# Kernel tuning notes

Measured on AMD Instinct MI355X. Metric: run time of the kernel, lower is better.

The kernel has to match this reference:

```python
import jax, jax.numpy as jnp
import numpy as np

N_AGENT = 32768   # number of agent (dst) nodes
MAX_NBRS = 16     # fixed neighbor count per agent (pad target)
N_NBR = N_AGENT * MAX_NBRS   # nbr (src) nodes
E = N_AGENT * MAX_NBRS       # 1hop edges (grouped by dst)
F_NBR, F_AGENT, F_HOP = 32, 32, 8
H = 128           # critic_hidden_size
N_POW = 4         # n_pow_opts


def _lin(key, fin, fout):
    return jax.random.normal(key, (fin, fout), jnp.float32) / np.sqrt(fin)


def setup_inputs() -> dict:
    key = jax.random.key(0)
    ks = jax.random.split(key, 12)
    return {
        "feat_nbr": jax.random.normal(ks[0], (N_NBR, F_NBR), jnp.float32),
        "feat_agent": jax.random.normal(ks[1], (N_AGENT, F_AGENT), jnp.float32),
        "edge_feat": jax.random.normal(ks[2], (E, F_HOP), jnp.float32),
        "h": jnp.zeros((N_AGENT, H), jnp.float32),
        # NodeGNBlock '1hop': message MLP + update MLP
        "W_msg": _lin(ks[3], F_NBR + F_HOP, H), "b_msg": jnp.zeros((H,), jnp.float32),
        "W_upd": _lin(ks[4], H + F_AGENT, H), "b_upd": jnp.zeros((H,), jnp.float32),
        # RnnLayer: GRUCell(H, H)
        "W_x": _lin(ks[5], H, 3 * H), "W_h": _lin(ks[6], H, 3 * H),
        "b_ih": jnp.zeros((3 * H,), jnp.float32), "b_hh": jnp.zeros((3 * H,), jnp.float32),
        # EdgeGNBlock f_out: edge MLP -> per-edge q over power options, plus agent head
        "W_e1": _lin(ks[7], F_NBR + H + F_HOP, H), "b_e1": jnp.zeros((H,), jnp.float32),
        "W_e2": _lin(ks[8], H, N_POW), "b_e2": jnp.zeros((N_POW,), jnp.float32),
        "W_a": _lin(ks[9], 2 * H, 1), "b_a": jnp.zeros((1,), jnp.float32),
        # graph: each agent has exactly MAX_NBRS incident edges, grouped by dst
        "src_idx": jax.random.randint(ks[10], (E,), 0, N_NBR),
        "dst_idx": jnp.repeat(jnp.arange(N_AGENT), MAX_NBRS),
    }


def reference(feat_nbr, feat_agent, edge_feat, h,
              W_msg, b_msg, W_upd, b_upd,
              W_x, W_h, b_ih, b_hh,
              W_e1, b_e1, W_e2, b_e2, W_a, b_a,
              src_idx, dst_idx):
    act = jax.nn.relu
    # --- NodeGNBlock '1hop': edge message -> sum-aggregate -> node update ---
    m = act(jnp.concatenate([feat_nbr[src_idx], edge_feat], axis=1) @ W_msg + b_msg)  # [E,H]
    agg = jax.ops.segment_sum(m, dst_idx, num_segments=N_AGENT, indices_are_sorted=True)  # [N,H]
    x = act(jnp.concatenate([agg, feat_agent], axis=1) @ W_upd + b_upd)  # [N,H]
    # --- RnnLayer: GRUCell step; output x == new hidden ---
    gi = x @ W_x + b_ih
    gh = h @ W_h + b_hh
    ir, iz, inn = jnp.split(gi, 3, axis=1)
    hr, hz, hn = jnp.split(gh, 3, axis=1)
    r = jax.nn.sigmoid(ir + hr)
    z = jax.nn.sigmoid(iz + hz)
    n = jnp.tanh(inn + r * hn)
    h_new = (1.0 - z) * n + z * h  # [N,H]
    # --- EdgeGNBlock f_out: per-edge q-values + per-agent scalar ---
    ze = act(jnp.concatenate([feat_nbr[src_idx], h_new[dst_idx], edge_feat], axis=1) @ W_e1 + b_e1)  # [E,H]
    nbr_out = ze @ W_e2 + b_e2  # [E, N_POW]
    agg2 = jax.ops.segment_sum(ze, dst_idx, num_segments=N_AGENT, indices_are_sorted=True)
    agent_out = jnp.concatenate([agg2, h_new], axis=1) @ W_a + b_a  # [N,1]
    # --- pad_edge_output: edges grouped by dst with fixed degree -> reshape ---
    padded_nbr_out = nbr_out.reshape(N_AGENT, MAX_NBRS * N_POW)
    q_vals = jnp.concatenate([padded_nbr_out, agent_out], axis=1)  # [N, MAX_NBRS*N_POW+1]
    return q_vals, h_new
```

## Files before the change

kernel.cpp:

```cpp
#include <hip/hip_runtime.h>

typedef _Float16 half_t;
typedef half_t half8 __attribute__((ext_vector_type(8)));
typedef half_t half4 __attribute__((ext_vector_type(4)));
typedef float f32x4 __attribute__((ext_vector_type(4)));

#define NAGENT 32768
#define MAXN   16
#define HD     128
#define QCOLS  65
#define QN     (NAGENT * QCOLS)
#define AGB    16
#define EPB    (AGB * MAXN)
#define QROWB  260

#define O_WMT   0
#define O_WE1E  8192
#define O_WE1H  16384
#define O_WUPD  32768
#define O_WX    53248
#define O_WH    102400
#define W_TOTAL 151552

#define MFMA(a, b, c) __builtin_amdgcn_mfma_f32_16x16x32_f16((a), (b), (c), 0, 0, 0)

__global__ void prep_weights(const float* __restrict__ W_msg, const float* __restrict__ W_upd,
                             const float* __restrict__ W_x, const float* __restrict__ W_h,
                             const float* __restrict__ W_e1, half_t* __restrict__ ws) {
    int i = blockIdx.x * 256 + threadIdx.x;
    if (i >= W_TOTAL) return;
    float v; int dst;
    if (i < 8192) {
        int k = i >> 7, n = i & 127;
        v = (k < 40) ? W_msg[k * HD + n] : 0.f;
        dst = O_WMT + n * 64 + k;
    } else if (i < 16384) {
        int j = i - 8192; int k = j >> 7, n = j & 127;
        v = (k < 32) ? W_e1[k * HD + n] : (k < 40 ? W_e1[(160 + k - 32) * HD + n] : 0.f);
        dst = O_WE1E + n * 64 + k;
    } else if (i < 32768) {
        int j = i - 16384; int k = j >> 7, n = j & 127;
        v = W_e1[(32 + k) * HD + n];
        dst = O_WE1H + n * 128 + k;
    } else if (i < 53248) {
        int j = i - 32768; int k = j >> 7, n = j & 127;
        v = W_upd[k * HD + n];
        dst = O_WUPD + n * 160 + k;
    } else if (i < 102400) {
        int j = i - 53248; int k = j / 384, n = j - k * 384;
        v = W_x[k * 384 + n];
        dst = O_WX + n * 128 + k;
    } else {
        int j = i - 102400; int k = j / 384, n = j - k * 384;
        v = W_h[k * 384 + n];
        dst = O_WH + n * 128 + k;
    }
    ws[dst] = (half_t)v;
}

__device__ __forceinline__ half8 ldB(const half_t* __restrict__ WT, int kstride, int n0, int k0, int l) {
    return *(const half8*)(WT + (size_t)(n0 + (l & 15)) * kstride + k0 + ((l >> 4) * 8));
}
__device__ __forceinline__ half4 cvt4(float4 v) {
    return (half4){(half_t)v.x, (half_t)v.y, (half_t)v.z, (half_t)v.w};
}
__device__ __forceinline__ half8 cvt8(float4 a, float4 b) {
    return (half8){(half_t)a.x, (half_t)a.y, (half_t)a.z, (half_t)a.w,
                   (half_t)b.x, (half_t)b.y, (half_t)b.z, (half_t)b.w};
}
__device__ __forceinline__ float sigm(float x) { return 1.f / (1.f + __expf(-x)); }
__device__ __forceinline__ float tanh_fast(float x) { return 1.f - 2.f / (__expf(2.f * x) + 1.f); }

__global__ __launch_bounds__(256, 2) void k_msg(
    const float* __restrict__ feat_nbr, const float* __restrict__ edge_feat,
    const float* __restrict__ b_msg, const int* __restrict__ src_idx,
    const half_t* __restrict__ ws, float* __restrict__ out)
{
    const int t = threadIdx.x;
    const int w = t >> 6, l = t & 63;
    const int l16 = l & 15, q = l >> 4;
    const int a0 = blockIdx.x * AGB;
    const int be = blockIdx.x * EPB;
    const half_t* wmT = ws + O_WMT;
    const half8 hz = {0, 0, 0, 0, 0, 0, 0, 0};

    __shared__ int srcs[EPB];
    srcs[t] = src_idx[be + t];
    __syncthreads();

    half8 B[4][4];
    float bm0[4], bm1[4];
    #pragma unroll
    for (int nc = 0; nc < 4; ++nc) {
        const int n0 = nc * 32;
        B[nc][0] = ldB(wmT, 64, n0, 0, l);
        B[nc][1] = ldB(wmT, 64, n0, 32, l);
        B[nc][2] = ldB(wmT, 64, n0 + 16, 0, l);
        B[nc][3] = ldB(wmT, 64, n0 + 16, 32, l);
        bm0[nc] = b_msg[n0 + l16];
        bm1[nc] = b_msg[n0 + 16 + l16];
    }
    #pragma unroll
    for (int mt = 0; mt < 4; ++mt) {
        const int al = w * 4 + mt;
        const int arow = al * 16 + l16;
        const float* fr = feat_nbr + (size_t)srcs[arow] * 32 + q * 8;
        half8 af0 = cvt8(*(const float4*)fr, *(const float4*)(fr + 4));
        half8 af1 = hz;
        if (q == 0) {
            const float* er = edge_feat + (size_t)(be + arow) * 8;
            af1 = cvt8(*(const float4*)er, *(const float4*)(er + 4));
        }
        half_t* arow_out = (half_t*)((char*)out + (size_t)(a0 + al) * QROWB);
        #pragma unroll
        for (int nc = 0; nc < 4; ++nc) {
            f32x4 c0 = {0.f, 0.f, 0.f, 0.f}, c1 = {0.f, 0.f, 0.f, 0.f};
            c0 = MFMA(af0, B[nc][0], c0);
            c0 = MFMA(af1, B[nc][1], c0);
            c1 = MFMA(af0, B[nc][2], c1);
            c1 = MFMA(af1, B[nc][3], c1);
            float s0 = 0.f, s1 = 0.f;
            #pragma unroll
            for (int r = 0; r < 4; ++r) {
                s0 += fmaxf(c0[r] + bm0[nc], 0.f);
                s1 += fmaxf(c1[r] + bm1[nc], 0.f);
            }
            s0 += __shfl_xor(s0, 16); s0 += __shfl_xor(s0, 32);
            s1 += __shfl_xor(s1, 16); s1 += __shfl_xor(s1, 32);
            if (l < 16) {
                arow_out[nc * 32 + l] = (half_t)s0;
                arow_out[nc * 32 + 16 + l] = (half_t)s1;
            }
        }
    }
}

__global__ __launch_bounds__(256, 2) void k_node(
    const float* __restrict__ feat_agent, const float* __restrict__ h_in,
    const float* __restrict__ b_upd, const float* __restrict__ b_ih,
    const float* __restrict__ b_hh, const float* __restrict__ b_e1,
    const float* __restrict__ W_a, half_t* __restrict__ ws,
    float* __restrict__ out)
{
    const int t = threadIdx.x;
    const int w = t >> 6, l = t & 63;
    const int l16 = l & 15, q = l >> 4;
    const int a0 = blockIdx.x * AGB;
    const half_t* wupdT = ws + O_WUPD;
    const half_t* wxT   = ws + O_WX;
    const half_t* whT   = ws + O_WH;
    const half_t* we1hT = ws + O_WE1H;
    float* hn_wa_g = (float*)(ws + W_TOTAL);

    __shared__ half_t A2[AGB][168];
    __shared__ half_t h_lds[AGB][136];
    __shared__ half_t x_lds[AGB][136];
    __shared__ half_t hn_lds[AGB][136];
    __shared__ float  hnwa[AGB];

    if (t < AGB) hnwa[t] = 0.f;
    {
        int r = t >> 4, c = t & 15;
        half8 v = *(const half8*)((const char*)out + (size_t)(a0 + r) * QROWB + c * 16);
        *(half8*)&A2[r][c * 8] = v;
    }
    if (t < 128) {
        int r = t >> 3, p = t & 7;
        float4 v = ((const float4*)(feat_agent + (size_t)(a0 + r) * 32))[p];
        *(half4*)&A2[r][128 + p * 4] = cvt4(v);
    }
    #pragma unroll
    for (int i = 0; i < 2; ++i) {
        int g = t + 256 * i; int r = g >> 5, c = g & 31;
        float4 v = ((const float4*)(h_in + (size_t)(a0 + r) * HD))[c];
        *(half4*)&h_lds[r][c * 4] = cvt4(v);
    }
    __syncthreads();

    {
        half8 af[5];
        #pragma unroll
        for (int k = 0; k < 5; ++k) af[k] = *(const half8*)&A2[l16][k * 32 + q * 8];
        #pragma unroll
        for (int s = 0; s < 2; ++s) {
            const int n0 = (w * 2 + s) * 16;
            f32x4 c = {0.f, 0.f, 0.f, 0.f};
            #pragma unroll
            for (int k = 0; k < 5; ++k) c = MFMA(af[k], ldB(wupdT, 160, n0, k * 32, l), c);
            float bu = b_upd[n0 + l16];
            #pragma unroll
            for (int r = 0; r < 4; ++r)
                x_lds[q * 4 + r][n0 + l16] = (half_t)fmaxf(c[r] + bu, 0.f);
        }
    }
    __syncthreads();

    {
        half8 ax[4], ah[4];
        #pragma unroll
        for (int k = 0; k < 4; ++k) {
            ax[k] = *(const half8*)&x_lds[l16][k * 32 + q * 8];
            ah[k] = *(const half8*)&h_lds[l16][k * 32 + q * 8];
        }
        float pa[4] = {0.f, 0.f, 0.f, 0.f};
        #pragma unroll
        for (int s = 0; s < 2; ++s) {
            const int colb = w * 32 + s * 16;
            f32x4 gi[3], gh[3];
            #pragma unroll
            for (int g = 0; g < 3; ++g) {
                const int n0 = g * 128 + colb;
                f32x4 ci = {0.f, 0.f, 0.f, 0.f}, ch = {0.f, 0.f, 0.f, 0.f};
                #pragma unroll
                for (int k = 0; k < 4; ++k) {
                    ci = MFMA(ax[k], ldB(wxT, 128, n0, k * 32, l), ci);
                    ch = MFMA(ah[k], ldB(whT, 128, n0, k * 32, l), ch);
                }
                gi[g] = ci; gh[g] = ch;
            }
            const int col = colb + l16;
            float bi0 = b_ih[col], bi1 = b_ih[HD + col], bi2 = b_ih[2 * HD + col];
            float bh0 = b_hh[col], bh1 = b_hh[HD + col], bh2 = b_hh[2 * HD + col];
            float wac = W_a[HD + col];
            #pragma unroll
            for (int r = 0; r < 4; ++r) {
                const int row = q * 4 + r;
                float rg = sigm(gi[0][r] + bi0 + gh[0][r] + bh0);
                float zg = sigm(gi[1][r] + bi1 + gh[1][r] + bh1);
                float ng = tanh_fast(gi[2][r] + bi2 + rg * (gh[2][r] + bh2));
                float hv = (1.f - zg) * ng + zg * (float)h_lds[row][col];
                out[QN + (size_t)(a0 + row) * HD + col] = hv;
                hn_lds[row][col] = (half_t)hv;
                pa[r] = fmaf(hv, wac, pa[r]);
            }
        }
        #pragma unroll
        for (int r = 0; r < 4; ++r) {
            #pragma unroll
            for (int m = 1; m <= 8; m <<= 1) pa[r] += __shfl_xor(pa[r], m);
            if (l16 == 0) atomicAdd(&hnwa[q * 4 + r], pa[r]);
        }
    }
    __syncthreads();

    {
        half8 an[4];
        #pragma unroll
        for (int k = 0; k < 4; ++k) an[k] = *(const half8*)&hn_lds[l16][k * 32 + q * 8];
        #pragma unroll
        for (int s = 0; s < 2; ++s) {
            const int n0 = (w * 2 + s) * 16;
            f32x4 c = {0.f, 0.f, 0.f, 0.f};
            #pragma unroll
            for (int k = 0; k < 4; ++k) c = MFMA(an[k], ldB(we1hT, 128, n0, k * 32, l), c);
            float bv = b_e1[n0 + l16];
            #pragma unroll
            for (int r = 0; r < 4; ++r) {
                half_t* arow_out = (half_t*)((char*)out + (size_t)(a0 + q * 4 + r) * QROWB);
                arow_out[n0 + l16] = (half_t)(c[r] + bv);
            }
        }
    }
    if (t < AGB) hn_wa_g[a0 + t] = hnwa[t];
}

__global__ __launch_bounds__(256, 2) void k_edge(
    const float* __restrict__ feat_nbr, const float* __restrict__ edge_feat,
    const float* __restrict__ W_e2, const float* __restrict__ b_e2,
    const float* __restrict__ W_a, const float* __restrict__ b_a,
    const int* __restrict__ src_idx, const half_t* __restrict__ ws,
    float* __restrict__ out)
{
    const int t = threadIdx.x;
    const int w = t >> 6, l = t & 63;
    const int l16 = l & 15, q = l >> 4;
    const int a0 = blockIdx.x * AGB;
    const int be = blockIdx.x * EPB;
    const half_t* we1eT = ws + O_WE1E;
    const float* hn_wa_g = (const float*)(ws + W_TOTAL);
    const half8 hz = {0, 0, 0, 0, 0, 0, 0, 0};

    __shared__ int srcs[EPB];
    srcs[t] = src_idx[be + t];
    __syncthreads();

    half8 B[4][4];
    float wa0[4], wa1[4];
    #pragma unroll
    for (int nc = 0; nc < 4; ++nc) {
        const int n0 = nc * 32;
        B[nc][0] = ldB(we1eT, 64, n0, 0, l);
        B[nc][1] = ldB(we1eT, 64, n0, 32, l);
        B[nc][2] = ldB(we1eT, 64, n0 + 16, 0, l);
        B[nc][3] = ldB(we1eT, 64, n0 + 16, 32, l);
        wa0[nc] = W_a[n0 + l16];
        wa1[nc] = W_a[n0 + 16 + l16];
    }
    const float ba = b_a[0];

    #pragma unroll
    for (int mt = 0; mt < 4; ++mt) {
        const int al = w * 4 + mt;
        const int arow = al * 16 + l16;
        const float* fr = feat_nbr + (size_t)srcs[arow] * 32 + q * 8;
        half8 af0 = cvt8(*(const float4*)fr, *(const float4*)(fr + 4));
        half8 af1 = hz;
        if (q == 0) {
            const float* er = edge_feat + (size_t)(be + arow) * 8;
            af1 = cvt8(*(const float4*)er, *(const float4*)(er + 4));
        }
        const half_t* che_row = (const half_t*)((const char*)out + (size_t)(a0 + al) * QROWB);
        float qa[4][4];
        #pragma unroll
        for (int r = 0; r < 4; ++r)
            #pragma unroll
            for (int p = 0; p < 4; ++p) qa[r][p] = 0.f;
        float wa_part = 0.f;
        #pragma unroll
        for (int nc = 0; nc < 4; ++nc) {
            const int n0 = nc * 32;
            f32x4 c0 = {0.f, 0.f, 0.f, 0.f}, c1 = {0.f, 0.f, 0.f, 0.f};
            c0 = MFMA(af0, B[nc][0], c0);
            c0 = MFMA(af1, B[nc][1], c0);
            c1 = MFMA(af0, B[nc][2], c1);
            c1 = MFMA(af1, B[nc][3], c1);
            const int col0 = n0 + l16, col1 = n0 + 16 + l16;
            float ch0 = (float)che_row[col0], ch1 = (float)che_row[col1];
            float4 w20 = *(const float4*)(W_e2 + col0 * 4);
            float4 w21 = *(const float4*)(W_e2 + col1 * 4);
            float s0 = 0.f, s1 = 0.f;
            #pragma unroll
            for (int r = 0; r < 4; ++r) {
                float z0 = fmaxf(c0[r] + ch0, 0.f);
                float z1 = fmaxf(c1[r] + ch1, 0.f);
                s0 += z0; s1 += z1;
                qa[r][0] = fmaf(z0, w20.x, fmaf(z1, w21.x, qa[r][0]));
                qa[r][1] = fmaf(z0, w20.y, fmaf(z1, w21.y, qa[r][1]));
                qa[r][2] = fmaf(z0, w20.z, fmaf(z1, w21.z, qa[r][2]));
                qa[r][3] = fmaf(z0, w20.w, fmaf(z1, w21.w, qa[r][3]));
            }
            s0 += __shfl_xor(s0, 16); s0 += __shfl_xor(s0, 32);
            s1 += __shfl_xor(s1, 16); s1 += __shfl_xor(s1, 32);
            wa_part = fmaf(s0, wa0[nc], fmaf(s1, wa1[nc], wa_part));
        }
        #pragma unroll
        for (int m = 1; m <= 8; m <<= 1)
            #pragma unroll
            for (int r = 0; r < 4; ++r)
                #pragma unroll
                for (int p = 0; p < 4; ++p) qa[r][p] += __shfl_xor(qa[r][p], m);
        if (l16 < 4) {
            const int p = l16;
            const float bz = b_e2[p];
            #pragma unroll
            for (int r = 0; r < 4; ++r)
                out[(size_t)(a0 + al) * QCOLS + (q * 4 + r) * 4 + p] = qa[r][p] + bz;
        }
        #pragma unroll
        for (int m = 1; m <= 8; m <<= 1) wa_part += __shfl_xor(wa_part, m);
        if (l == 0)
            out[(size_t)(a0 + al) * QCOLS + 64] = wa_part + hn_wa_g[a0 + al] + ba;
    }
}

extern "C" void kernel_launch(void* const* d_in, const int* in_sizes, int n_in,
                              void* d_out, int out_size, void* d_ws, size_t ws_size,
                              hipStream_t stream) {
    const float* feat_nbr   = (const float*)d_in[0];
    const float* feat_agent = (const float*)d_in[1];
    const float* edge_feat  = (const float*)d_in[2];
    const float* h_in       = (const float*)d_in[3];
    const float* W_msg = (const float*)d_in[4];
    const float* b_msg = (const float*)d_in[5];
    const float* W_upd = (const float*)d_in[6];
    const float* b_upd = (const float*)d_in[7];
    const float* W_x   = (const float*)d_in[8];
    const float* W_h   = (const float*)d_in[9];
    const float* b_ih  = (const float*)d_in[10];
    const float* b_hh  = (const float*)d_in[11];
    const float* W_e1  = (const float*)d_in[12];
    const float* b_e1  = (const float*)d_in[13];
    const float* W_e2  = (const float*)d_in[14];
    const float* b_e2  = (const float*)d_in[15];
    const float* W_a   = (const float*)d_in[16];
    const float* b_a   = (const float*)d_in[17];
    const int* src_idx = (const int*)d_in[18];
    half_t* ws = (half_t*)d_ws;
    float* out = (float*)d_out;
    const int nblk = NAGENT / AGB;

    prep_weights<<<(W_TOTAL + 255) / 256, 256, 0, stream>>>(W_msg, W_upd, W_x, W_h, W_e1, ws);
    k_msg<<<nblk, 256, 0, stream>>>(feat_nbr, edge_feat, b_msg, src_idx, ws, out);
    k_node<<<nblk, 256, 0, stream>>>(feat_agent, h_in, b_upd, b_ih, b_hh, b_e1, W_a, ws, out);
    k_edge<<<nblk, 256, 0, stream>>>(feat_nbr, edge_feat, W_e2, b_e2, W_a, b_a, src_idx, ws, out);
}
```

Baseline: 316.1 us.

## Fuse message, node/GRU and edge kernels into one per-block kernel

Merges the three per-block kernels (k_msg, k_node, k_edge) into a single kernel. Intermediates (aggregated messages, h_new projections, the hn·W_a partial) now stay in LDS instead of round-tripping through the output buffer and workspace. The gathered feat_nbr and edge_feat rows are cached in LDS as fp16 and reused by the edge stage, so the random gather happens once instead of twice. LDS buffers are aliased to limit shared memory, and launch bounds are raised to 3 blocks per CU. The risks are higher register and LDS pressure and a longer serial dependency chain within each block.

```diff
diff --git a/kernel.cpp b/kernel.cpp
--- a/kernel.cpp
+++ b/kernel.cpp
@@ -12,7 +12,6 @@
 #define QN     (NAGENT * QCOLS)
 #define AGB    16
 #define EPB    (AGB * MAXN)
-#define QROWB  260
 
 #define O_WMT   0
 #define O_WE1E  8192
@@ -71,9 +70,14 @@
 __device__ __forceinline__ float sigm(float x) { return 1.f / (1.f + __expf(-x)); }
 __device__ __forceinline__ float tanh_fast(float x) { return 1.f - 2.f / (__expf(2.f * x) + 1.f); }
 
-__global__ __launch_bounds__(256, 2) void k_msg(
-    const float* __restrict__ feat_nbr, const float* __restrict__ edge_feat,
-    const float* __restrict__ b_msg, const int* __restrict__ src_idx,
+__global__ __launch_bounds__(256, 3) void k_fused(
+    const float* __restrict__ feat_nbr, const float* __restrict__ feat_agent,
+    const float* __restrict__ edge_feat, const float* __restrict__ h_in,
+    const float* __restrict__ b_msg, const float* __restrict__ b_upd,
+    const float* __restrict__ b_ih, const float* __restrict__ b_hh,
+    const float* __restrict__ b_e1, const float* __restrict__ W_e2,
+    const float* __restrict__ b_e2, const float* __restrict__ W_a,
+    const float* __restrict__ b_a, const int* __restrict__ src_idx,
     const half_t* __restrict__ ws, float* __restrict__ out)
 {
     const int t = threadIdx.x;
@@ -81,93 +85,21 @@
     const int l16 = l & 15, q = l >> 4;
     const int a0 = blockIdx.x * AGB;
     const int be = blockIdx.x * EPB;
-    const half_t* wmT = ws + O_WMT;
     const half8 hz = {0, 0, 0, 0, 0, 0, 0, 0};
 
-    __shared__ int srcs[EPB];
+    __shared__ int    srcs[EPB];
+    __shared__ half_t fnef[EPB][40];
+    __shared__ half_t bufA[AGB][168];
+    __shared__ half_t h_lds[AGB][136];
+    __shared__ half_t bufB[AGB][136];
+    __shared__ float  hnwa[AGB];
+
     srcs[t] = src_idx[be + t];
-    __syncthreads();
-
-    half8 B[4][4];
-    float bm0[4], bm1[4];
-    #pragma unroll
-    for (int nc = 0; nc < 4; ++nc) {
-        const int n0 = nc * 32;
-        B[nc][0] = ldB(wmT, 64, n0, 0, l);
-        B[nc][1] = ldB(wmT, 64, n0, 32, l);
-        B[nc][2] = ldB(wmT, 64, n0 + 16, 0, l);
-        B[nc][3] = ldB(wmT, 64, n0 + 16, 32, l);
-        bm0[nc] = b_msg[n0 + l16];
-        bm1[nc] = b_msg[n0 + 16 + l16];
-    }
-    #pragma unroll
-    for (int mt = 0; mt < 4; ++mt) {
-        const int al = w * 4 + mt;
-        const int arow = al * 16 + l16;
-        const float* fr = feat_nbr + (size_t)srcs[arow] * 32 + q * 8;
-        half8 af0 = cvt8(*(const float4*)fr, *(const float4*)(fr + 4));
-        half8 af1 = hz;
-        if (q == 0) {
-            const float* er = edge_feat + (size_t)(be + arow) * 8;
-            af1 = cvt8(*(const float4*)er, *(const float4*)(er + 4));
-        }
-        half_t* arow_out = (half_t*)((char*)out + (size_t)(a0 + al) * QROWB);
-        #pragma unroll
-        for (int nc = 0; nc < 4; ++nc) {
-            f32x4 c0 = {0.f, 0.f, 0.f, 0.f}, c1 = {0.f, 0.f, 0.f, 0.f};
-            c0 = MFMA(af0, B[nc][0], c0);
-            c0 = MFMA(af1, B[nc][1], c0);
-            c1 = MFMA(af0, B[nc][2], c1);
-            c1 = MFMA(af1, B[nc][3], c1);
-            float s0 = 0.f, s1 = 0.f;
-            #pragma unroll
-            for (int r = 0; r < 4; ++r) {
-                s0 += fmaxf(c0[r] + bm0[nc], 0.f);
-                s1 += fmaxf(c1[r] + bm1[nc], 0.f);
-            }
-            s0 += __shfl_xor(s0, 16); s0 += __shfl_xor(s0, 32);
-            s1 += __shfl_xor(s1, 16); s1 += __shfl_xor(s1, 32);
-            if (l < 16) {
-                arow_out[nc * 32 + l] = (half_t)s0;
-                arow_out[nc * 32 + 16 + l] = (half_t)s1;
-            }
-        }
-    }
-}
-
-__global__ __launch_bounds__(256, 2) void k_node(
-    const float* __restrict__ feat_agent, const float* __restrict__ h_in,
-    const float* __restrict__ b_upd, const float* __restrict__ b_ih,
-    const float* __restrict__ b_hh, const float* __restrict__ b_e1,
-    const float* __restrict__ W_a, half_t* __restrict__ ws,
-    float* __restrict__ out)
-{
-    const int t = threadIdx.x;
-    const int w = t >> 6, l = t & 63;
-    const int l16 = l & 15, q = l >> 4;
-    const int a0 = blockIdx.x * AGB;
-    const half_t* wupdT = ws + O_WUPD;
-    const half_t* wxT   = ws + O_WX;
-    const half_t* whT   = ws + O_WH;
-    const half_t* we1hT = ws + O_WE1H;
-    float* hn_wa_g = (float*)(ws + W_TOTAL);
-
-    __shared__ half_t A2[AGB][168];
-    __shared__ half_t h_lds[AGB][136];
-    __shared__ half_t x_lds[AGB][136];
-    __shared__ half_t hn_lds[AGB][136];
-    __shared__ float  hnwa[AGB];
-
     if (t < AGB) hnwa[t] = 0.f;
-    {
-        int r = t >> 4, c = t & 15;
-        half8 v = *(const half8*)((const char*)out + (size_t)(a0 + r) * QROWB + c * 16);
-        *(half8*)&A2[r][c * 8] = v;
-    }
     if (t < 128) {
         int r = t >> 3, p = t & 7;
         float4 v = ((const float4*)(feat_agent + (size_t)(a0 + r) * 32))[p];
-        *(half4*)&A2[r][128 + p * 4] = cvt4(v);
+        *(half4*)&bufA[r][128 + p * 4] = cvt4(v);
     }
     #pragma unroll
     for (int i = 0; i < 2; ++i) {
@@ -178,9 +110,61 @@
     __syncthreads();
 
     {
+        const half_t* wmT = ws + O_WMT;
+        half8 B[4][4];
+        float bm0[4], bm1[4];
+        #pragma unroll
+        for (int nc = 0; nc < 4; ++nc) {
+            const int n0 = nc * 32;
+            B[nc][0] = ldB(wmT, 64, n0, 0, l);
+            B[nc][1] = ldB(wmT, 64, n0, 32, l);
+            B[nc][2] = ldB(wmT, 64, n0 + 16, 0, l);
+            B[nc][3] = ldB(wmT, 64, n0 + 16, 32, l);
+            bm0[nc] = b_msg[n0 + l16];
+            bm1[nc] = b_msg[n0 + 16 + l16];
+        }
+        #pragma unroll
+        for (int mt = 0; mt < 4; ++mt) {
+            const int al = w * 4 + mt;
+            const int arow = al * 16 + l16;
+            const float* fr = feat_nbr + (size_t)srcs[arow] * 32 + q * 8;
+            half8 af0 = cvt8(*(const float4*)fr, *(const float4*)(fr + 4));
+            half8 af1 = hz;
+            if (q == 0) {
+                const float* er = edge_feat + (size_t)(be + arow) * 8;
+                af1 = cvt8(*(const float4*)er, *(const float4*)(er + 4));
+            }
+            *(half8*)&fnef[arow][q * 8] = af0;
+            if (q == 0) *(half8*)&fnef[arow][32] = af1;
+            #pragma unroll
+            for (int nc = 0; nc < 4; ++nc) {
+                f32x4 c0 = {0.f, 0.f, 0.f, 0.f}, c1 = {0.f, 0.f, 0.f, 0.f};
+                c0 = MFMA(af0, B[nc][0], c0);
+                c0 = MFMA(af1, B[nc][1], c0);
+                c1 = MFMA(af0, B[nc][2], c1);
+                c1 = MFMA(af1, B[nc][3], c1);
+                float s0 = 0.f, s1 = 0.f;
+                #pragma unroll
+                for (int r = 0; r < 4; ++r) {
+                    s0 += fmaxf(c0[r] + bm0[nc], 0.f);
+                    s1 += fmaxf(c1[r] + bm1[nc], 0.f);
+                }
+                s0 += __shfl_xor(s0, 16); s0 += __shfl_xor(s0, 32);
+                s1 += __shfl_xor(s1, 16); s1 += __shfl_xor(s1, 32);
+                if (l < 16) {
+                    bufA[al][nc * 32 + l]      = (half_t)s0;
+                    bufA[al][nc * 32 + 16 + l] = (half_t)s1;
+                }
+            }
+        }
+    }
+    __syncthreads();
+
+    {
+        const half_t* wupdT = ws + O_WUPD;
         half8 af[5];
         #pragma unroll
-        for (int k = 0; k < 5; ++k) af[k] = *(const half8*)&A2[l16][k * 32 + q * 8];
+        for (int k = 0; k < 5; ++k) af[k] = *(const half8*)&bufA[l16][k * 32 + q * 8];
         #pragma unroll
         for (int s = 0; s < 2; ++s) {
             const int n0 = (w * 2 + s) * 16;
@@ -190,16 +174,18 @@
             float bu = b_upd[n0 + l16];
             #pragma unroll
             for (int r = 0; r < 4; ++r)
-                x_lds[q * 4 + r][n0 + l16] = (half_t)fmaxf(c[r] + bu, 0.f);
-        }
-    }
-    __syncthreads();
-
-    {
+                bufB[q * 4 + r][n0 + l16] = (half_t)fmaxf(c[r] + bu, 0.f);
+        }
+    }
+    __syncthreads();
+
+    {
+        const half_t* wxT = ws + O_WX;
+        const half_t* whT = ws + O_WH;
         half8 ax[4], ah[4];
         #pragma unroll
         for (int k = 0; k < 4; ++k) {
-            ax[k] = *(const half8*)&x_lds[l16][k * 32 + q * 8];
+            ax[k] = *(const half8*)&bufB[l16][k * 32 + q * 8];
             ah[k] = *(const half8*)&h_lds[l16][k * 32 + q * 8];
         }
         float pa[4] = {0.f, 0.f, 0.f, 0.f};
@@ -230,7 +216,7 @@
                 float ng = tanh_fast(gi[2][r] + bi2 + rg * (gh[2][r] + bh2));
                 float hv = (1.f - zg) * ng + zg * (float)h_lds[row][col];
                 out[QN + (size_t)(a0 + row) * HD + col] = hv;
-                hn_lds[row][col] = (half_t)hv;
+                bufA[row][col] = (half_t)hv;
                 pa[r] = fmaf(hv, wac, pa[r]);
             }
         }
@@ -244,9 +230,10 @@
     __syncthreads();
 
     {
+        const half_t* we1hT = ws + O_WE1H;
         half8 an[4];
         #pragma unroll
-        for (int k = 0; k < 4; ++k) an[k] = *(const half8*)&hn_lds[l16][k * 32 + q * 8];
+        for (int k = 0; k < 4; ++k) an[k] = *(const half8*)&bufA[l16][k * 32 + q * 8];
         #pragma unroll
         for (int s = 0; s < 2; ++s) {
             const int n0 = (w * 2 + s) * 16;
@@ -255,111 +242,86 @@
             for (int k = 0; k < 4; ++k) c = MFMA(an[k], ldB(we1hT, 128, n0, k * 32, l), c);
             float bv = b_e1[n0 + l16];
             #pragma unroll
-            for (int r = 0; r < 4; ++r) {
-                half_t* arow_out = (half_t*)((char*)out + (size_t)(a0 + q * 4 + r) * QROWB);
-                arow_out[n0 + l16] = (half_t)(c[r] + bv);
-            }
-        }
-    }
-    if (t < AGB) hn_wa_g[a0 + t] = hnwa[t];
-}
-
-__global__ __launch_bounds__(256, 2) void k_edge(
-    const float* __restrict__ feat_nbr, const float* __restrict__ edge_feat,
-    const float* __restrict__ W_e2, const float* __restrict__ b_e2,
-    const float* __restrict__ W_a, const float* __restrict__ b_a,
-    const int* __restrict__ src_idx, const half_t* __restrict__ ws,
-    float* __restrict__ out)
-{
-    const int t = threadIdx.x;
-    const int w = t >> 6, l = t & 63;
-    const int l16 = l & 15, q = l >> 4;
-    const int a0 = blockIdx.x * AGB;
-    const int be = blockIdx.x * EPB;
-    const half_t* we1eT = ws + O_WE1E;
-    const float* hn_wa_g = (const float*)(ws + W_TOTAL);
-    const half8 hz = {0, 0, 0, 0, 0, 0, 0, 0};
-
-    __shared__ int srcs[EPB];
-    srcs[t] = src_idx[be + t];
-    __syncthreads();
-
-    half8 B[4][4];
-    float wa0[4], wa1[4];
-    #pragma unroll
-    for (int nc = 0; nc < 4; ++nc) {
-        const int n0 = nc * 32;
-        B[nc][0] = ldB(we1eT, 64, n0, 0, l);
-        B[nc][1] = ldB(we1eT, 64, n0, 32, l);
-        B[nc][2] = ldB(we1eT, 64, n0 + 16, 0, l);
-        B[nc][3] = ldB(we1eT, 64, n0 + 16, 32, l);
-        wa0[nc] = W_a[n0 + l16];
-        wa1[nc] = W_a[n0 + 16 + l16];
-    }
-    const float ba = b_a[0];
-
-    #pragma unroll
-    for (int mt = 0; mt < 4; ++mt) {
-        const int al = w * 4 + mt;
-        const int arow = al * 16 + l16;
-        const float* fr = feat_nbr + (size_t)srcs[arow] * 32 + q * 8;
-        half8 af0 = cvt8(*(const float4*)fr, *(const float4*)(fr + 4));
-        half8 af1 = hz;
-        if (q == 0) {
-            const float* er = edge_feat + (size_t)(be + arow) * 8;
-            af1 = cvt8(*(const float4*)er, *(const float4*)(er + 4));
-        }
-        const half_t* che_row = (const half_t*)((const char*)out + (size_t)(a0 + al) * QROWB);
-        float qa[4][4];
-        #pragma unroll
-        for (int r = 0; r < 4; ++r)
-            #pragma unroll
-            for (int p = 0; p < 4; ++p) qa[r][p] = 0.f;
-        float wa_part = 0.f;
+            for (int r = 0; r < 4; ++r)
+                bufB[q * 4 + r][n0 + l16] = (half_t)(c[r] + bv);
+        }
+    }
+    __syncthreads();
+
+    {
+        const half_t* we1eT = ws + O_WE1E;
+        half8 B[4][4];
+        float wa0[4], wa1[4];
         #pragma unroll
         for (int nc = 0; nc < 4; ++nc) {
             const int n0 = nc * 32;
-            f32x4 c0 = {0.f, 0.f, 0.f, 0.f}, c1 = {0.f, 0.f, 0.f, 0.f};
-            c0 = MFMA(af0, B[nc][0], c0);
-            c0 = MFMA(af1, B[nc][1], c0);
-            c1 = MFMA(af0, B[nc][2], c1);
-            c1 = MFMA(af1, B[nc][3], c1);
-            const int col0 = n0 + l16, col1 = n0 + 16 + l16;
-            float ch0 = (float)che_row[col0], ch1 = (float)che_row[col1];
-            float4 w20 = *(const float4*)(W_e2 + col0 * 4);
-            float4 w21 = *(const float4*)(W_e2 + col1 * 4);
-            float s0 = 0.f, s1 = 0.f;
-            #pragma unroll
-            for (int r = 0; r < 4; ++r) {
-                float z0 = fmaxf(c0[r] + ch0, 0.f);
-                float z1 = fmaxf(c1[r] + ch1, 0.f);
-                s0 += z0; s1 += z1;
-                qa[r][0] = fmaf(z0, w20.x, fmaf(z1, w21.x, qa[r][0]));
-                qa[r][1] = fmaf(z0, w20.y, fmaf(z1, w21.y, qa[r][1]));
-                qa[r][2] = fmaf(z0, w20.z, fmaf(z1, w21.z, qa[r][2]));
-                qa[r][3] = fmaf(z0, w20.w, fmaf(z1, w21.w, qa[r][3]));
-            }
-            s0 += __shfl_xor(s0, 16); s0 += __shfl_xor(s0, 32);
-            s1 += __shfl_xor(s1, 16); s1 += __shfl_xor(s1, 32);
-            wa_part = fmaf(s0, wa0[nc], fmaf(s1, wa1[nc], wa_part));
-        }
-        #pragma unroll
-        for (int m = 1; m <= 8; m <<= 1)
+            B[nc][0] = ldB(we1eT, 64, n0, 0, l);
+            B[nc][1] = ldB(we1eT, 64, n0, 32, l);
+            B[nc][2] = ldB(we1eT, 64, n0 + 16, 0, l);
+            B[nc][3] = ldB(we1eT, 64, n0 + 16, 32, l);
+            wa0[nc] = W_a[n0 + l16];
+            wa1[nc] = W_a[n0 + 16 + l16];
+        }
+        const float ba = b_a[0];
+
+        #pragma unroll
+        for (int mt = 0; mt < 4; ++mt) {
+            const int al = w * 4 + mt;
+            const int arow = al * 16 + l16;
+            half8 af0 = *(const half8*)&fnef[arow][q * 8];
+            half8 af1 = hz;
+            if (q == 0) af1 = *(const half8*)&fnef[arow][32];
+            float qa[4][4];
             #pragma unroll
             for (int r = 0; r < 4; ++r)
                 #pragma unroll
-                for (int p = 0; p < 4; ++p) qa[r][p] += __shfl_xor(qa[r][p], m);
-        if (l16 < 4) {
-            const int p = l16;
-            const float bz = b_e2[p];
-            #pragma unroll
-            for (int r = 0; r < 4; ++r)
-                out[(size_t)(a0 + al) * QCOLS + (q * 4 + r) * 4 + p] = qa[r][p] + bz;
-        }
-        #pragma unroll
-        for (int m = 1; m <= 8; m <<= 1) wa_part += __shfl_xor(wa_part, m);
-        if (l == 0)
-            out[(size_t)(a0 + al) * QCOLS + 64] = wa_part + hn_wa_g[a0 + al] + ba;
+                for (int p = 0; p < 4; ++p) qa[r][p] = 0.f;
+            float wa_part = 0.f;
+            #pragma unroll
+            for (int nc = 0; nc < 4; ++nc) {
+                const int n0 = nc * 32;
+                f32x4 c0 = {0.f, 0.f, 0.f, 0.f}, c1 = {0.f, 0.f, 0.f, 0.f};
+                c0 = MFMA(af0, B[nc][0], c0);
+                c0 = MFMA(af1, B[nc][1], c0);
+                c1 = MFMA(af0, B[nc][2], c1);
+                c1 = MFMA(af1, B[nc][3], c1);
+                const int col0 = n0 + l16, col1 = n0 + 16 + l16;
+                float ch0 = (float)bufB[al][col0], ch1 = (float)bufB[al][col1];
+                float4 w20 = *(const float4*)(W_e2 + col0 * 4);
+                float4 w21 = *(const float4*)(W_e2 + col1 * 4);
+                float s0 = 0.f, s1 = 0.f;
+                #pragma unroll
+                for (int r = 0; r < 4; ++r) {
+                    float z0 = fmaxf(c0[r] + ch0, 0.f);
+                    float z1 = fmaxf(c1[r] + ch1, 0.f);
+                    s0 += z0; s1 += z1;
+                    qa[r][0] = fmaf(z0, w20.x, fmaf(z1, w21.x, qa[r][0]));
+                    qa[r][1] = fmaf(z0, w20.y, fmaf(z1, w21.y, qa[r][1]));
+                    qa[r][2] = fmaf(z0, w20.z, fmaf(z1, w21.z, qa[r][2]));
+                    qa[r][3] = fmaf(z0, w20.w, fmaf(z1, w21.w, qa[r][3]));
+                }
+                s0 += __shfl_xor(s0, 16); s0 += __shfl_xor(s0, 32);
+                s1 += __shfl_xor(s1, 16); s1 += __shfl_xor(s1, 32);
+                wa_part = fmaf(s0, wa0[nc], fmaf(s1, wa1[nc], wa_part));
+            }
+            #pragma unroll
+            for (int m = 1; m <= 8; m <<= 1)
+                #pragma unroll
+                for (int r = 0; r < 4; ++r)
+                    #pragma unroll
+                    for (int p = 0; p < 4; ++p) qa[r][p] += __shfl_xor(qa[r][p], m);
+            if (l16 < 4) {
+                const int p = l16;
+                const float bz = b_e2[p];
+                #pragma unroll
+                for (int r = 0; r < 4; ++r)
+                    out[(size_t)(a0 + al) * QCOLS + (q * 4 + r) * 4 + p] = qa[r][p] + bz;
+            }
+            #pragma unroll
+            for (int m = 1; m <= 8; m <<= 1) wa_part += __shfl_xor(wa_part, m);
+            if (l == 0)
+                out[(size_t)(a0 + al) * QCOLS + 64] = wa_part + hnwa[al] + ba;
+        }
     }
 }
 
@@ -390,7 +352,7 @@
     const int nblk = NAGENT / AGB;
 
     prep_weights<<<(W_TOTAL + 255) / 256, 256, 0, stream>>>(W_msg, W_upd, W_x, W_h, W_e1, ws);
-    k_msg<<<nblk, 256, 0, stream>>>(feat_nbr, edge_feat, b_msg, src_idx, ws, out);
-    k_node<<<nblk, 256, 0, stream>>>(feat_agent, h_in, b_upd, b_ih, b_hh, b_e1, W_a, ws, out);
-    k_edge<<<nblk, 256, 0, stream>>>(feat_nbr, edge_feat, W_e2, b_e2, W_a, b_a, src_idx, ws, out);
-}
+    k_fused<<<nblk, 256, 0, stream>>>(feat_nbr, feat_agent, edge_feat, h_in,
+                                      b_msg, b_upd, b_ih, b_hh, b_e1,
+                                      W_e2, b_e2, W_a, b_a, src_idx, ws, out);
+}
```

Result: slower. 344.3 us (+8.9%).
